# Optimization experiments

Hardware: AMD Instinct MI355X
Metric: run time of the kernel (lower is better)

Reference implementation:

```python
import jax, jax.numpy as jnp
import numpy as np
import math

D_MODEL = 1024
N_HEADS = 16
B, S = 4, 2048

def _xavier(key, shape):
    fan_out, fan_in = shape
    limit = math.sqrt(6.0 / (fan_in + fan_out))
    return jax.random.uniform(key, shape, jnp.float32, -limit, limit)

def setup_inputs() -> dict:
    key = jax.random.key(0)
    kx, kqkv, ko = jax.random.split(key, 3)
    x = jax.random.normal(kx, (B, S, D_MODEL), dtype=jnp.float32)
    W_qkv = _xavier(kqkv, (3 * D_MODEL, D_MODEL))
    W_o = _xavier(ko, (D_MODEL, D_MODEL))
    return {"x": x, "W_qkv": W_qkv, "W_o": W_o}

def reference(x, W_qkv, W_o):
    Bx, Sx, D = x.shape
    H = N_HEADS
    d_h = D // H
    T = jnp.einsum('bsd,ed->bse', x, W_qkv)          # (B,S,3D)
    Q, K, V = jnp.split(T, 3, axis=-1)
    # (B,S,D) -> (B,H,S,d_h)
    Q = Q.reshape(Bx, Sx, H, d_h).transpose(0, 2, 1, 3)
    K = K.reshape(Bx, Sx, H, d_h).transpose(0, 2, 1, 3)
    V = V.reshape(Bx, Sx, H, d_h).transpose(0, 2, 1, 3)
    scores = jnp.einsum('bhqd,bhkd->bhqk', Q, K) / jnp.sqrt(jnp.float32(d_h))
    attn = jax.nn.softmax(scores, axis=-1)
    out = jnp.einsum('bhqk,bhkd->bhqd', attn, V)
    out = out.transpose(0, 2, 1, 3).reshape(Bx, Sx, D)
    Y = jnp.einsum('bsd,ed->bse', out, W_o)
    return Y
```

## Files before the change

### kernel.cpp

```cpp
#include <hip/hip_runtime.h>
#include <stdint.h>

#define SS 2048

typedef __attribute__((ext_vector_type(8))) short short8;
typedef __attribute__((ext_vector_type(4))) float f32x4;
typedef __attribute__((ext_vector_type(16))) float f32x16;

static __device__ __forceinline__ unsigned short f2bf(float f) {
    uint32_t u = __builtin_bit_cast(uint32_t, f);
    u += 0x7fffu + ((u >> 16) & 1u);
    return (unsigned short)(u >> 16);
}

static __device__ __forceinline__ uint32_t cvtpk(float lo, float hi) {
    uint32_t r;
    asm("v_cvt_pk_bf16_f32 %0, %1, %2" : "=v"(r) : "v"(lo), "v"(hi));
    return r;
}

static __device__ __forceinline__ void async16(const unsigned short* g, unsigned short* l) {
    __builtin_amdgcn_global_load_lds(
        (const __attribute__((address_space(1))) uint32_t*)g,
        (__attribute__((address_space(3))) uint32_t*)l, 16, 0, 0);
}

__global__ void cast_f32_bf16(const float* __restrict__ src, unsigned short* __restrict__ dst, int n) {
    int i = (blockIdx.x * 256 + threadIdx.x) * 4;
    if (i >= n) return;
    float4 v = *(const float4*)(src + i);
    ushort4 o;
    o.x = f2bf(v.x); o.y = f2bf(v.y); o.z = f2bf(v.z); o.w = f2bf(v.w);
    *(ushort4*)(dst + i) = o;
}

template<int MODE>
__global__ void gemm_bt(const unsigned short* __restrict__ A,
                        const unsigned short* __restrict__ Bm,
                        void* __restrict__ Cout,
                        unsigned short* __restrict__ Vt,
                        int K) {
    __shared__ unsigned short As[128 * 64];
    __shared__ unsigned short Bs[128 * 64];
    const int t = threadIdx.x;
    const int w = t >> 6, l = t & 63;
    const int wm = w >> 1, wn = w & 1;
    const int l15 = l & 15, l4 = l >> 4;
    const int m0 = blockIdx.x * 128, n0 = blockIdx.y * 128;
    const int srow = t >> 3;
    const int scol = (t & 7) * 8;

    f32x4 acc[4][4] = {};

    for (int k0 = 0; k0 < K; k0 += 64) {
#pragma unroll
        for (int r = 0; r < 4; ++r) {
            int row = r * 32 + srow;
            async16(A + (size_t)(m0 + row) * K + k0 + scol, (unsigned short*)&As[row * 64 + scol]);
        }
#pragma unroll
        for (int r = 0; r < 4; ++r) {
            int row = r * 32 + srow;
            async16(Bm + (size_t)(n0 + row) * K + k0 + scol, (unsigned short*)&Bs[row * 64 + scol]);
        }
        __syncthreads();
#pragma unroll
        for (int kk = 0; kk < 64; kk += 32) {
            short8 af[4], bfr[4];
#pragma unroll
            for (int m = 0; m < 4; ++m)
                af[m] = *(const short8*)&As[(wm * 64 + m * 16 + l15) * 64 + kk + l4 * 8];
#pragma unroll
            for (int n = 0; n < 4; ++n)
                bfr[n] = *(const short8*)&Bs[(wn * 64 + n * 16 + l15) * 64 + kk + l4 * 8];
#pragma unroll
            for (int m = 0; m < 4; ++m)
#pragma unroll
                for (int n = 0; n < 4; ++n)
                    acc[m][n] = __builtin_amdgcn_mfma_f32_16x16x32_bf16(af[m], bfr[n], acc[m][n], 0, 0, 0);
        }
        __syncthreads();
    }

#pragma unroll
    for (int m = 0; m < 4; ++m) {
        int rbase = m0 + wm * 64 + m * 16 + l4 * 4;
#pragma unroll
        for (int n = 0; n < 4; ++n) {
            int c = n0 + wn * 64 + n * 16 + l15;
            f32x4 v = acc[m][n];
            if (MODE == 0) {
                if (c < 2048) {
                    float sc = (c < 1024) ? 0.18033688f : 1.0f;
                    unsigned short* T = (unsigned short*)Cout;
#pragma unroll
                    for (int r = 0; r < 4; ++r)
                        T[(size_t)(rbase + r) * 2048 + c] = f2bf(v[0 + r] * sc);
                } else {
                    int vv = c - 2048;
                    int hh = vv >> 6, d = vv & 63;
                    int bb = rbase >> 11, s = rbase & 2047;
                    ushort4 pk;
                    pk.x = f2bf(v[0]); pk.y = f2bf(v[1]); pk.z = f2bf(v[2]); pk.w = f2bf(v[3]);
                    *(ushort4*)&Vt[((size_t)(bb * 16 + hh) * 64 + d) * 2048 + s] = pk;
                }
            } else {
                float* C = (float*)Cout;
#pragma unroll
                for (int r = 0; r < 4; ++r)
                    C[(size_t)(rbase + r) * 1024 + c] = v[r];
            }
        }
    }
}

__global__ __launch_bounds__(256, 4) void attn_kernel(
        const unsigned short* __restrict__ Tqk,
        const unsigned short* __restrict__ Vt,
        unsigned short* __restrict__ Out) {
    __shared__ unsigned short Ks[2][64 * 64];
    __shared__ unsigned short Vs[2][64 * 64];
    const int t = threadIdx.x;
    const int w = t >> 6, l = t & 63;
    const int lq = l & 31, hfl = l >> 5;

    const int lin = blockIdx.x;
    const int j = lin >> 3;
    const int bh = (lin & 7) * 8 + (j & 7);
    const int qt = j >> 3;
    const int b = bh >> 4, hh = bh & 15;
    const int qrow = qt * 128 + w * 32 + lq;

    short8 qf[4];
    const size_t trow = ((size_t)b * SS + qrow) * 2048;
#pragma unroll
    for (int dc = 0; dc < 4; ++dc)
        qf[dc] = *(const short8*)&Tqk[trow + hh * 64 + dc * 16 + hfl * 8];

    char* KsB = (char*)Ks;
    char* VsB = (char*)Vs;

    const int srow = t >> 3;
    const int scb = (t & 7) << 4;
    const int ssw = scb ^ ((srow & 7) << 4);
    const int sel = scb >> 1;

    const unsigned short* kp0 = Tqk + (size_t)b * SS * 2048 + 1024 + hh * 64 + (size_t)srow * 2048 + sel;
    const unsigned short* kp1 = kp0 + 32 * 2048;
    const unsigned short* vp0 = Vt + (size_t)bh * 64 * 2048 + (size_t)srow * 2048 + sel;
    const unsigned short* vp1 = vp0 + 32 * 2048;

    int4 kr0, kr1, vr0, vr1;
#define ISSUE()                                                                      \
    kr0 = *(const int4*)kp0; kr1 = *(const int4*)kp1;                                \
    vr0 = *(const int4*)vp0; vr1 = *(const int4*)vp1;
#define WRITE(buf)                                                                   \
    {                                                                                \
        char* kb = KsB + (buf) * 8192;                                               \
        char* vb = VsB + (buf) * 8192;                                               \
        *(int4*)(kb + srow * 128 + ssw) = kr0;                                       \
        *(int4*)(kb + (srow + 32) * 128 + ssw) = kr1;                                \
        *(int4*)(vb + srow * 128 + ssw) = vr0;                                       \
        *(int4*)(vb + (srow + 32) * 128 + ssw) = vr1;                                \
    }

    f32x16 oacc[2] = {};
    float la0 = 0.f, la1 = 0.f, la2 = 0.f, la3 = 0.f;

    ISSUE();
    WRITE(0);
    __syncthreads();

    for (int it = 0; it < 32; ++it) {
        const int cur = it & 1;
        const char* kb = KsB + cur * 8192;
        const char* vb = VsB + cur * 8192;
        const bool more = (it < 31);
        if (more) {
            kp0 += 64 * 2048; kp1 += 64 * 2048;
            vp0 += 64;        vp1 += 64;
            ISSUE();
        }

        f32x16 sa[2] = {};
        __builtin_amdgcn_s_setprio(1);
#pragma unroll
        for (int kvt = 0; kvt < 2; ++kvt) {
            int row = kvt * 32 + lq;
#pragma unroll
            for (int dc = 0; dc < 4; ++dc) {
                short8 kf = *(const short8*)(kb + row * 128 + ((dc * 32 + hfl * 16) ^ ((row & 7) << 4)));
                sa[kvt] = __builtin_amdgcn_mfma_f32_32x32x16_bf16(kf, qf[dc], sa[kvt], 0, 0, 0);
            }
        }
        __builtin_amdgcn_s_setprio(0);

#pragma unroll
        for (int kvt = 0; kvt < 2; ++kvt)
#pragma unroll
            for (int r = 0; r < 16; r += 4) {
                float p0 = __builtin_amdgcn_exp2f(sa[kvt][r + 0]);
                float p1 = __builtin_amdgcn_exp2f(sa[kvt][r + 1]);
                float p2 = __builtin_amdgcn_exp2f(sa[kvt][r + 2]);
                float p3 = __builtin_amdgcn_exp2f(sa[kvt][r + 3]);
                sa[kvt][r + 0] = p0; la0 += p0;
                sa[kvt][r + 1] = p1; la1 += p1;
                sa[kvt][r + 2] = p2; la2 += p2;
                sa[kvt][r + 3] = p3; la3 += p3;
            }

        short8 pb[4];
#pragma unroll
        for (int c = 0; c < 4; ++c) {
            int f = c >> 1, r0 = (c & 1) * 8;
            uint32_t v0 = cvtpk(sa[f][r0 + 0], sa[f][r0 + 1]);
            uint32_t v1 = cvtpk(sa[f][r0 + 2], sa[f][r0 + 3]);
            uint32_t v2 = cvtpk(sa[f][r0 + 4], sa[f][r0 + 5]);
            uint32_t v3 = cvtpk(sa[f][r0 + 6], sa[f][r0 + 7]);
            asm("v_permlane32_swap_b32 %0, %1" : "+v"(v0), "+v"(v2));
            asm("v_permlane32_swap_b32 %0, %1" : "+v"(v1), "+v"(v3));
            union { uint32_t u[4]; short8 s; } pbu;
            pbu.u[0] = v0;
            pbu.u[1] = v1;
            pbu.u[2] = v2;
            pbu.u[3] = v3;
            pb[c] = pbu.s;
        }

        __builtin_amdgcn_s_setprio(1);
#pragma unroll
        for (int dt = 0; dt < 2; ++dt) {
            int row0 = dt * 32 + lq;
#pragma unroll
            for (int c = 0; c < 4; ++c) {
                short8 vf = *(const short8*)(vb + row0 * 128 + ((c * 32 + hfl * 16) ^ ((row0 & 7) << 4)));
                oacc[dt] = __builtin_amdgcn_mfma_f32_32x32x16_bf16(vf, pb[c], oacc[dt], 0, 0, 0);
            }
        }
        __builtin_amdgcn_s_setprio(0);

        if (more) { WRITE(cur ^ 1); }
        __syncthreads();
    }
#undef ISSUE
#undef WRITE

    float l_run = (la0 + la1) + (la2 + la3);
    l_run += __shfl_xor(l_run, 32);
    float inv = 1.0f / l_run;
    const size_t obase = ((size_t)b * SS + qrow) * 1024 + hh * 64;
#pragma unroll
    for (int dt = 0; dt < 2; ++dt)
#pragma unroll
        for (int r = 0; r < 16; ++r) {
            int d = dt * 32 + (r & 3) + 8 * (r >> 2) + 4 * hfl;
            Out[obase + d] = f2bf(oacc[dt][r] * inv);
        }
}

extern "C" void kernel_launch(void* const* d_in, const int* in_sizes, int n_in,
                              void* d_out, int out_size, void* d_ws, size_t ws_size,
                              hipStream_t stream) {
    const float* x    = (const float*)d_in[0];
    const float* wqkv = (const float*)d_in[1];
    const float* wo   = (const float*)d_in[2];

    unsigned short* ws  = (unsigned short*)d_ws;
    unsigned short* xb  = ws;
    unsigned short* w1  = ws + 8388608;
    unsigned short* w2  = ws + 11534336;
    unsigned short* vt  = ws + 12582912;
    unsigned short* ao  = ws + 20971520;
    unsigned short* tqk = (unsigned short*)d_out;

    cast_f32_bf16<<<8192, 256, 0, stream>>>(x, xb, 8388608);
    cast_f32_bf16<<<3072, 256, 0, stream>>>(wqkv, w1, 3145728);
    cast_f32_bf16<<<1024, 256, 0, stream>>>(wo, w2, 1048576);

    gemm_bt<0><<<dim3(64, 24), 256, 0, stream>>>(xb, w1, (void*)tqk, vt, 1024);
    attn_kernel<<<1024, 256, 0, stream>>>(tqk, vt, ao);
    gemm_bt<1><<<dim3(64, 8), 256, 0, stream>>>(ao, w2, d_out, nullptr, 1024);
}
```

Before: 190.4 us.

## Replace QKV projection GEMM with 256x256-tile double-buffered pipelined kernel

```diff
diff --git a/kernel.cpp b/kernel.cpp
--- a/kernel.cpp
+++ b/kernel.cpp
@@ -34,12 +34,131 @@
     *(ushort4*)(dst + i) = o;
 }
 
-template<int MODE>
+__global__ __launch_bounds__(512, 2) void gemm256_qkv(
+        const unsigned short* __restrict__ A,
+        const unsigned short* __restrict__ B,
+        unsigned short* __restrict__ Tqk,
+        unsigned short* __restrict__ Vt) {
+    extern __shared__ char sm[];
+    const int t = threadIdx.x, w = t >> 6, l = t & 63;
+    const int wm = w >> 2, wn = w & 3;
+    const int l15 = l & 15, l4 = l >> 4;
+    const int lr = l >> 3, lc = l & 7;
+
+    const int lin = blockIdx.x;
+    const int wg = (lin & 7) * 48 + (lin >> 3);
+    const int bm = wg & 31, bn = wg >> 5;
+    const int m0 = bm * 256, n0 = bn * 256;
+
+    const int u_a = wn;
+    const int u_b = wm * 2 + (wn & 1);
+    const int scol = (lc ^ lr) * 8;
+
+    const unsigned short* Ab = A + (size_t)(m0 + wm * 128 + u_a * 8 + lr) * 1024 + scol;
+    const unsigned short* Bb = B + (size_t)(n0 + (wn >> 1) * 128 + u_b * 8 + lr) * 1024 + scol;
+
+    char* const smA = sm + wm * 16384;
+    char* const smB = sm + 32768 + (wn >> 1) * 16384;
+    const int adst = (u_a * 8 + lr) * 128 + lc * 16;
+    const int bdst = (u_b * 8 + lr) * 128 + lc * 16;
+
+#define SA(j, T, buf) async16(Ab + (j) * 32768 + (size_t)(T) * 64, \
+        (unsigned short*)(smA + (buf) * 65536 + (j) * 4096 + adst))
+#define SB(j, T, buf) async16(Bb + (size_t)((((j) & 1) * 64 + ((j) >> 1) * 32)) * 1024 + (size_t)(T) * 64, \
+        (unsigned short*)(smB + (buf) * 65536 + ((((j) & 1) * 64 + ((j) >> 1) * 32)) * 128 + bdst))
+
+    const int rc0 = ((0 + l4) ^ (l15 & 7)) * 16;
+    const int rc1 = ((4 + l4) ^ (l15 & 7)) * 16;
+    const int arow = l15 * 128;
+    const int brow = ((wn & 1) * 64 + l15) * 128;
+
+    f32x4 acc[8][4] = {};
+    short8 af[4][2], bfr[2][2];
+
+#define RD_A(lo) { const char* Ar = smA + cur * 65536 + (lo) * 8192 + arow;          \
+    af[0][0] = *(const short8*)(Ar + 0 * 2048 + rc0);                                \
+    af[0][1] = *(const short8*)(Ar + 0 * 2048 + rc1);                                \
+    af[1][0] = *(const short8*)(Ar + 1 * 2048 + rc0);                                \
+    af[1][1] = *(const short8*)(Ar + 1 * 2048 + rc1);                                \
+    af[2][0] = *(const short8*)(Ar + 2 * 2048 + rc0);                                \
+    af[2][1] = *(const short8*)(Ar + 2 * 2048 + rc1);                                \
+    af[3][0] = *(const short8*)(Ar + 3 * 2048 + rc0);                                \
+    af[3][1] = *(const short8*)(Ar + 3 * 2048 + rc1); }
+#define RD_B(hi) { const char* Br = smB + cur * 65536 + brow + (hi) * 4096;          \
+    bfr[0][0] = *(const short8*)(Br + 0 * 2048 + rc0);                               \
+    bfr[0][1] = *(const short8*)(Br + 0 * 2048 + rc1);                               \
+    bfr[1][0] = *(const short8*)(Br + 1 * 2048 + rc0);                               \
+    bfr[1][1] = *(const short8*)(Br + 1 * 2048 + rc1); }
+#define MM(R, C) _Pragma("unroll") for (int m = 0; m < 4; ++m)                       \
+    _Pragma("unroll") for (int n = 0; n < 2; ++n) {                                  \
+        acc[(R)*4+m][(C)*2+n] = __builtin_amdgcn_mfma_f32_16x16x32_bf16(             \
+            af[m][0], bfr[n][0], acc[(R)*4+m][(C)*2+n], 0, 0, 0);                    \
+        acc[(R)*4+m][(C)*2+n] = __builtin_amdgcn_mfma_f32_16x16x32_bf16(             \
+            af[m][1], bfr[n][1], acc[(R)*4+m][(C)*2+n], 0, 0, 0); }
+#define VM4 asm volatile("s_waitcnt vmcnt(4)" ::: "memory")
+#define BAR __builtin_amdgcn_s_barrier()
+#define SP1 __builtin_amdgcn_s_setprio(1)
+#define SP0 __builtin_amdgcn_s_setprio(0)
+
+    SA(0, 0, 0); SA(1, 0, 0); SB(0, 0, 0); SB(1, 0, 0);
+    SA(2, 0, 0); SA(3, 0, 0); SB(2, 0, 0); SB(3, 0, 0);
+
+    for (int tt = 0; tt < 16; ++tt) {
+        const int cur = tt & 1, nxt = cur ^ 1;
+        const int Tn = (tt + 1 < 16) ? tt + 1 : 0;
+        VM4; BAR;
+        RD_A(0); RD_B(0);
+        SA(0, Tn, nxt); SA(1, Tn, nxt);
+        SP1; MM(0, 0); SP0; BAR;
+        VM4; BAR;
+        RD_A(1);
+        SB(0, Tn, nxt); SB(1, Tn, nxt);
+        SP1; MM(1, 0); SP0; BAR;
+        VM4; BAR;
+        RD_B(1);
+        SA(2, Tn, nxt); SA(3, Tn, nxt);
+        SP1; MM(1, 1); SP0; BAR;
+        RD_A(0);
+        SB(2, Tn, nxt); SB(3, Tn, nxt);
+        SP1; MM(0, 1); SP0; BAR;
+    }
+#undef SA
+#undef SB
+#undef RD_A
+#undef RD_B
+#undef MM
+#undef VM4
+#undef BAR
+#undef SP1
+#undef SP0
+
+#pragma unroll
+    for (int fm = 0; fm < 8; ++fm) {
+        int rbase = m0 + wm * 128 + fm * 16 + l4 * 4;
+#pragma unroll
+        for (int fn = 0; fn < 4; ++fn) {
+            int c = n0 + wn * 64 + fn * 16 + l15;
+            f32x4 v = acc[fm][fn];
+            if (c < 2048) {
+                float sc = (c < 1024) ? 0.18033688f : 1.0f;
+#pragma unroll
+                for (int r = 0; r < 4; ++r)
+                    Tqk[(size_t)(rbase + r) * 2048 + c] = f2bf(v[r] * sc);
+            } else {
+                int vv = c - 2048;
+                int hh = vv >> 6, d = vv & 63;
+                int bb = rbase >> 11, s = rbase & 2047;
+                ushort4 pk;
+                pk.x = f2bf(v[0]); pk.y = f2bf(v[1]); pk.z = f2bf(v[2]); pk.w = f2bf(v[3]);
+                *(ushort4*)&Vt[((size_t)(bb * 16 + hh) * 64 + d) * 2048 + s] = pk;
+            }
+        }
+    }
+}
+
 __global__ void gemm_bt(const unsigned short* __restrict__ A,
                         const unsigned short* __restrict__ Bm,
-                        void* __restrict__ Cout,
-                        unsigned short* __restrict__ Vt,
-                        int K) {
+                        float* __restrict__ C, int K) {
     __shared__ unsigned short As[128 * 64];
     __shared__ unsigned short Bs[128 * 64];
     const int t = threadIdx.x;
@@ -89,27 +208,9 @@
         for (int n = 0; n < 4; ++n) {
             int c = n0 + wn * 64 + n * 16 + l15;
             f32x4 v = acc[m][n];
-            if (MODE == 0) {
-                if (c < 2048) {
-                    float sc = (c < 1024) ? 0.18033688f : 1.0f;
-                    unsigned short* T = (unsigned short*)Cout;
-#pragma unroll
-                    for (int r = 0; r < 4; ++r)
-                        T[(size_t)(rbase + r) * 2048 + c] = f2bf(v[0 + r] * sc);
-                } else {
-                    int vv = c - 2048;
-                    int hh = vv >> 6, d = vv & 63;
-                    int bb = rbase >> 11, s = rbase & 2047;
-                    ushort4 pk;
-                    pk.x = f2bf(v[0]); pk.y = f2bf(v[1]); pk.z = f2bf(v[2]); pk.w = f2bf(v[3]);
-                    *(ushort4*)&Vt[((size_t)(bb * 16 + hh) * 64 + d) * 2048 + s] = pk;
-                }
-            } else {
-                float* C = (float*)Cout;
-#pragma unroll
-                for (int r = 0; r < 4; ++r)
-                    C[(size_t)(rbase + r) * 1024 + c] = v[r];
-            }
+#pragma unroll
+            for (int r = 0; r < 4; ++r)
+                C[(size_t)(rbase + r) * 1024 + c] = v[r];
         }
     }
 }
@@ -273,11 +374,14 @@
     unsigned short* ao  = ws + 20971520;
     unsigned short* tqk = (unsigned short*)d_out;
 
+    (void)hipFuncSetAttribute((const void*)gemm256_qkv,
+                              hipFuncAttributeMaxDynamicSharedMemorySize, 131072);
+
     cast_f32_bf16<<<8192, 256, 0, stream>>>(x, xb, 8388608);
     cast_f32_bf16<<<3072, 256, 0, stream>>>(wqkv, w1, 3145728);
     cast_f32_bf16<<<1024, 256, 0, stream>>>(wo, w2, 1048576);
 
-    gemm_bt<0><<<dim3(64, 24), 256, 0, stream>>>(xb, w1, (void*)tqk, vt, 1024);
+    gemm256_qkv<<<384, 512, 131072, stream>>>(xb, w1, tqk, vt);
     attn_kernel<<<1024, 256, 0, stream>>>(tqk, vt, ao);
-    gemm_bt<1><<<dim3(64, 8), 256, 0, stream>>>(ao, w2, d_out, nullptr, 1024);
-}
+    gemm_bt<<<dim3(64, 8), 256, 0, stream>>>(ao, w2, (float*)d_out, 1024);
+}
```

Result: no change. 194.2 us (+2.0%).
